# Optimization experiments

Measured on AMD Instinct MI355X. Metric: run time of the kernel, lower is better.

## Reference

```python
import jax, jax.numpy as jnp
import numpy as np

B, NF, DIM, H, W = 2, 8, 128, 40, 40
HID = 256
INNER = 2 * HID            # expansion=2
QKB = 4                    # qkv_block_size -> head dim
NH = INNER // QKB          # 128 heads
DH = QKB                   # 4


def _layernorm(x, w, b, eps=1e-5):
    mu = x.mean(-1, keepdims=True)
    var = x.var(-1, keepdims=True)
    return (x - mu) / jnp.sqrt(var + eps) * w + b


def _mlstm(q, k, v, ig, fg):
    # q,k,v: (Bp,NH,S,DH); ig,fg: (Bp,NH,S,1). Parallel stabilized mLSTM.
    S = q.shape[2]
    lfc = jnp.cumsum(jax.nn.log_sigmoid(fg), axis=2)            # (Bp,NH,S,1)
    m = lfc - jnp.swapaxes(lfc, -2, -1)                          # (Bp,NH,S,S): lfc[i]-lfc[j]
    tri = jnp.tril(jnp.ones((S, S), dtype=bool))
    logD = jnp.where(tri, m + jnp.swapaxes(ig, -2, -1), -jnp.inf)
    maxD = jnp.max(logD, axis=-1, keepdims=True)
    Dm = jnp.exp(logD - maxD)
    qk = jnp.einsum('bnsd,bntd->bnst', q, k) / jnp.sqrt(jnp.asarray(DH, q.dtype))
    C = qk * Dm
    normalizer = jnp.maximum(jnp.abs(C.sum(-1, keepdims=True)), jnp.exp(-maxD))
    return jnp.einsum('bnst,bntd->bnsd', C / (normalizer + 1e-6), v)


def _vil_layer(x, up_w, up_b, conv_w, conv_b, q_w, k_w, ig_w, ig_b, fg_w, fg_b, onorm_w, onorm_b, skip, down_w, down_b):
    Bp, S, _ = x.shape
    xz = x @ up_w.T + up_b                                       # (Bp,S,2*INNER)
    xm, z = jnp.split(xz, 2, axis=-1)
    # causal depthwise conv1d, kernel 4, left pad 3
    xc = jax.lax.conv_general_dilated(jnp.swapaxes(xm, 1, 2), conv_w[:, None, :], (1,), [(3, 0)],
                                      dimension_numbers=('NCH', 'OIH', 'NCH'), feature_group_count=INNER)
    xa = jax.nn.silu(jnp.swapaxes(xc, 1, 2) + conv_b)            # (Bp,S,INNER)
    xah = xa.reshape(Bp, S, NH, DH)
    qh = jnp.einsum('bsnd,ned->bsne', xah, q_w)                  # headwise linear (no bias)
    kh = jnp.einsum('bsnd,ned->bsne', xah, k_w)
    gate_in = jnp.concatenate([qh.reshape(Bp, S, INNER), kh.reshape(Bp, S, INNER), xm], axis=-1)
    ig = jnp.swapaxes(gate_in @ ig_w.T + ig_b, 1, 2)[..., None]  # (Bp,NH,S,1)
    fg = jnp.swapaxes(gate_in @ fg_w.T + fg_b, 1, 2)[..., None]
    q = jnp.swapaxes(qh, 1, 2)
    k = jnp.swapaxes(kh, 1, 2)
    v = jnp.swapaxes(xm.reshape(Bp, S, NH, DH), 1, 2)
    h = _mlstm(q, k, v, ig, fg)                                  # (Bp,NH,S,DH)
    mu = h.mean(-1, keepdims=True)
    var = h.var(-1, keepdims=True)
    hn = (h - mu) / jnp.sqrt(var + 1e-5) * onorm_w.reshape(NH, DH)[None, :, None, :] + onorm_b.reshape(NH, DH)[None, :, None, :]
    h_flat = jnp.swapaxes(hn, 1, 2).reshape(Bp, S, INNER)
    hs = h_flat + skip * xa
    return (hs * jax.nn.silu(z)) @ down_w.T + down_b


def _forward(x, in_fc1_w, in_fc1_b, in_fc2_w, in_fc2_b, out_fc1_w, out_fc1_b, out_fc2_w, out_fc2_b,
             norm_w, norm_b, up_w, up_b, conv_w, conv_b, q_w, k_w, ig_w, ig_b, fg_w, fg_b,
             onorm_w, onorm_b, skip, down_w, down_b):
    Bv, nf, C, Hh, Ww = x.shape
    x_flat = jnp.transpose(x, (0, 3, 4, 1, 2)).reshape(Bv * Hh * Ww, nf, C)
    h = jax.nn.gelu(x_flat @ in_fc1_w.T + in_fc1_b, approximate=False)
    h = h @ in_fc2_w.T + in_fc2_b
    # ViLBlockPair: forward-direction block then backward (flipped) block, each pre-LN residual
    for i, flip in ((0, False), (1, True)):
        y = _layernorm(h, norm_w[i], norm_b[i])
        if flip:
            y = y[:, ::-1]
        y = _vil_layer(y, up_w[i], up_b[i], conv_w[i], conv_b[i], q_w[i], k_w[i], ig_w[i], ig_b[i],
                       fg_w[i], fg_b[i], onorm_w[i], onorm_b[i], skip[i], down_w[i], down_b[i])
        if flip:
            y = y[:, ::-1]
        h = h + y
    o = jax.nn.gelu(h @ out_fc1_w.T + out_fc1_b, approximate=False)
    o = o @ out_fc2_w.T + out_fc2_b
    out = x_flat + o
    return jnp.transpose(out.reshape(Bv, Hh, Ww, nf, C), (0, 3, 4, 1, 2))


def setup_inputs() -> dict:
    key = jax.random.key(0)
    ks = jax.random.split(key, 16)

    def rn(k, shape, std=0.02):
        return jax.random.normal(k, shape, jnp.float32) * std

    return {
        'x': jax.random.normal(ks[0], (B, NF, DIM, H, W), jnp.float32),
        'in_fc1_w': rn(ks[1], (DIM, DIM)), 'in_fc1_b': jnp.zeros((DIM,), jnp.float32),
        'in_fc2_w': rn(ks[2], (HID, DIM)), 'in_fc2_b': jnp.zeros((HID,), jnp.float32),
        'out_fc1_w': rn(ks[3], (HID, HID)), 'out_fc1_b': jnp.zeros((HID,), jnp.float32),
        'out_fc2_w': rn(ks[4], (DIM, HID)), 'out_fc2_b': jnp.zeros((DIM,), jnp.float32),
        'norm_w': jnp.ones((2, HID), jnp.float32), 'norm_b': jnp.zeros((2, HID), jnp.float32),
        'up_w': rn(ks[5], (2, 2 * INNER, HID)), 'up_b': jnp.zeros((2, 2 * INNER), jnp.float32),
        'conv_w': rn(ks[6], (2, INNER, 4), 0.1), 'conv_b': jnp.zeros((2, INNER), jnp.float32),
        'q_w': rn(ks[7], (2, NH, DH, DH), 0.1), 'k_w': rn(ks[8], (2, NH, DH, DH), 0.1),
        'ig_w': rn(ks[9], (2, NH, 3 * INNER), 0.01), 'ig_b': rn(ks[10], (2, NH), 0.1),
        'fg_w': rn(ks[11], (2, NH, 3 * INNER), 0.01),
        'fg_b': jnp.tile(jnp.linspace(3.0, 6.0, NH, dtype=jnp.float32)[None], (2, 1)),
        'onorm_w': jnp.ones((2, INNER), jnp.float32), 'onorm_b': jnp.zeros((2, INNER), jnp.float32),
        'skip': jnp.ones((2, INNER), jnp.float32),
        'down_w': rn(ks[12], (2, HID, INNER)), 'down_b': jnp.zeros((2, HID), jnp.float32),
    }


def reference(x, in_fc1_w, in_fc1_b, in_fc2_w, in_fc2_b, out_fc1_w, out_fc1_b, out_fc2_w, out_fc2_b,
              norm_w, norm_b, up_w, up_b, conv_w, conv_b, q_w, k_w, ig_w, ig_b, fg_w, fg_b,
              onorm_w, onorm_b, skip, down_w, down_b):
    return _forward(x, in_fc1_w, in_fc1_b, in_fc2_w, in_fc2_b, out_fc1_w, out_fc1_b, out_fc2_w, out_fc2_b,
                    norm_w, norm_b, up_w, up_b, conv_w, conv_b, q_w, k_w, ig_w, ig_b, fg_w, fg_b,
                    onorm_w, onorm_b, skip, down_w, down_b)
```

## Files before the change

### kernel.cpp

```cpp
#include <hip/hip_runtime.h>
#include <cstddef>
#include <cstdint>


#define NPOS 3200
#define MTOK 25600

typedef __attribute__((ext_vector_type(8))) short short8;
typedef __attribute__((ext_vector_type(8))) unsigned short u16x8;
typedef __attribute__((ext_vector_type(4))) float f32x4;

__device__ __forceinline__ float bf2f(unsigned short u) {
  union { uint32_t i; float f; } v; v.i = ((uint32_t)u) << 16; return v.f;
}
__device__ __forceinline__ unsigned short f2bf(float f) {
  union { float f; uint32_t i; } v; v.f = f;
  uint32_t r = (v.i + 0x7fffu + ((v.i >> 16) & 1u)) >> 16;
  return (unsigned short)r;
}
__device__ __forceinline__ float geluf(float x) {
  return 0.5f * x * (1.0f + erff(x * 0.70710678118654752f));
}
__device__ __forceinline__ float fast_rcp(float x) { return __builtin_amdgcn_rcpf(x); }
__device__ __forceinline__ float silu_fast(float x) {
  return x * fast_rcp(1.0f + __expf(-x));
}

#define OFF_FC1 0
#define OFF_FC2 16384
#define OFF_OFC1 49152
#define OFF_OFC2 114688
#define OFF_UP 147456
#define OFF_DW 671744
#define OFF_GW 933888
#define WB_ELEMS 1458176

__global__ __launch_bounds__(256) void wprep(const float* __restrict__ fc1w,
                                             const float* __restrict__ fc2w,
                                             const float* __restrict__ ofc1w,
                                             const float* __restrict__ ofc2w,
                                             const float* __restrict__ upw,
                                             const float* __restrict__ dww,
                                             const float* __restrict__ igw,
                                             const float* __restrict__ fgw,
                                             const float* __restrict__ qw,
                                             const float* __restrict__ kw,
                                             const float* __restrict__ igbias,
                                             const float* __restrict__ fgbias,
                                             unsigned short* __restrict__ wb,
                                             float* __restrict__ gbias) {
  int i = blockIdx.x * 256 + threadIdx.x;
  if (i < 16384) { wb[OFF_FC1 + i] = f2bf(fc1w[i]); return; }
  i -= 16384;
  if (i < 32768) { wb[OFF_FC2 + i] = f2bf(fc2w[i]); return; }
  i -= 32768;
  if (i < 65536) { wb[OFF_OFC1 + i] = f2bf(ofc1w[i]); return; }
  i -= 65536;
  if (i < 32768) { wb[OFF_OFC2 + i] = f2bf(ofc2w[i]); return; }
  i -= 32768;
  if (i < 524288) { wb[OFF_UP + i] = f2bf(upw[i]); return; }
  i -= 524288;
  if (i < 262144) { wb[OFF_DW + i] = f2bf(dww[i]); return; }
  i -= 262144;
  if (i < 262144) {
    const int l = i >> 17;
    const int r = i & 131071;
    const int gate = r >> 16;
    const int rr = r & 65535;
    const int row = rr >> 9, c = rr & 511;
    const float* src = (gate ? fgw : igw) + (size_t)l * 196608 + (size_t)row * 1536 + 1024 + c;
    wb[OFF_GW + (size_t)l * 262144 + (size_t)(gate * 128 + row) * 1024 + 512 + c] = f2bf(*src);
    return;
  }
  i -= 262144;
  if (i < 131072) {
    const int l = i >> 16;
    const int r = i & 65535;
    const int jj = r >> 9, c = r & 511;
    const int n = c >> 2, d = c & 3;
    const float* igp = igw + (size_t)l * 196608;
    const float* fgp = fgw + (size_t)l * 196608;
    const float* qp = qw + l * 2048;
    const float* kp = kw + l * 2048;
    float si = 0.f, sf = 0.f;
#pragma unroll
    for (int e = 0; e < 4; ++e) {
      const float qv = qp[n * 16 + e * 4 + d];
      const float kv = kp[n * 16 + e * 4 + d];
      si += igp[jj * 1536 + n * 4 + e] * qv + igp[jj * 1536 + 512 + n * 4 + e] * kv;
      sf += fgp[jj * 1536 + n * 4 + e] * qv + fgp[jj * 1536 + 512 + n * 4 + e] * kv;
    }
    wb[OFF_GW + (size_t)l * 262144 + (size_t)jj * 1024 + c] = f2bf(si);
    wb[OFF_GW + (size_t)l * 262144 + (size_t)(128 + jj) * 1024 + c] = f2bf(sf);
    return;
  }
  i -= 131072;
  if (i < 512) {
    const int l = i >> 8, c = i & 255;
    gbias[l * 256 + c] = (c < 128) ? igbias[l * 128 + c] : fgbias[l * 128 + c - 128];
  }
}

__global__ __launch_bounds__(256) void trans_in(const float* __restrict__ x,
                                                unsigned short* __restrict__ xf) {
  __shared__ float tile[32][33];
  const int b = blockIdx.z;
  const int hw0 = blockIdx.x * 32;
  const int sc0 = blockIdx.y * 32;
  const int tx = threadIdx.x, ty = threadIdx.y;
#pragma unroll
  for (int i = 0; i < 32; i += 8)
    tile[ty + i][tx] = x[((size_t)b * 1024 + sc0 + ty + i) * 1600 + hw0 + tx];
  __syncthreads();
#pragma unroll
  for (int i = 0; i < 32; i += 8)
    xf[((size_t)b * 1600 + hw0 + ty + i) * 1024 + sc0 + tx] = f2bf(tile[tx][ty + i]);
}

__global__ __launch_bounds__(256) void trans_out(const float* __restrict__ x,
                                                 const unsigned short* __restrict__ o,
                                                 float* __restrict__ out) {
  __shared__ float tile[32][33];
  const int b = blockIdx.z;
  const int hw0 = blockIdx.x * 32;
  const int sc0 = blockIdx.y * 32;
  const int tx = threadIdx.x, ty = threadIdx.y;
#pragma unroll
  for (int i = 0; i < 32; i += 8)
    tile[ty + i][tx] = bf2f(o[((size_t)b * 1600 + hw0 + ty + i) * 1024 + sc0 + tx]);
  __syncthreads();
#pragma unroll
  for (int i = 0; i < 32; i += 8) {
    size_t idx = ((size_t)b * 1024 + sc0 + ty + i) * 1600 + hw0 + tx;
    out[idx] = x[idx] + tile[tx][ty + i];
  }
}

template <int MODE>
__global__ __launch_bounds__(256) void mgemm(const unsigned short* __restrict__ A, int lda,
                                             const unsigned short* __restrict__ A2, int lda2,
                                             int KA,
                                             const unsigned short* __restrict__ W, int ldw,
                                             const float* __restrict__ bias,
                                             const float* __restrict__ Cin,
                                             void* __restrict__ Cv, int ldc, int K,
                                             int flip) {
  __shared__ __align__(16) unsigned short Als[2][4][128][8];
  __shared__ __align__(16) unsigned short Bls[2][4][128][8];
  const int t = threadIdx.x;
  const int lane = t & 63, wid = t >> 6;
  const int wr = wid >> 1, wc = wid & 1;
  const int nwg = gridDim.x * gridDim.y;
  const int bid = blockIdx.y * gridDim.x + blockIdx.x;
  const int q = nwg >> 3, r = nwg & 7;
  const int xcd = bid & 7, idx = bid >> 3;
  const int swz = (xcd < r ? xcd * (q + 1) : r * (q + 1) + (xcd - r) * q) + idx;
  const int bx = swz & (gridDim.x - 1);
  const int by = swz >> (31 - __builtin_clz(gridDim.x));
  const int bm = by * 128, bn = bx * 128;
  const int srow = t >> 1;
  const int skh = (t & 1) << 4;
  const int ch = skh >> 3;
  const int kc = lane >> 4;
  const int lr = lane & 15;
  f32x4 acc[4][4] = {};
  const unsigned short* Wp = W + (size_t)(bn + srow) * ldw + skh;

  auto gload = [&](int k0, u16x8& a0, u16x8& a1, u16x8& b0, u16x8& b1) {
    const unsigned short* Ab;
    int kk, ldA;
    if (k0 < KA) { Ab = A; kk = k0; ldA = lda; }
    else { Ab = A2; kk = k0 - KA; ldA = lda2; }
    const unsigned short* ap = Ab + (size_t)(bm + srow) * ldA + kk + skh;
    a0 = *(const u16x8*)ap;
    a1 = *(const u16x8*)(ap + 8);
    b0 = *(const u16x8*)(Wp + k0);
    b1 = *(const u16x8*)(Wp + k0 + 8);
  };
  auto swrite = [&](int buf, u16x8 a0, u16x8 a1, u16x8 b0, u16x8 b1) {
    *(u16x8*)&Als[buf][ch][srow][0] = a0;
    *(u16x8*)&Als[buf][ch + 1][srow][0] = a1;
    *(u16x8*)&Bls[buf][ch][srow][0] = b0;
    *(u16x8*)&Bls[buf][ch + 1][srow][0] = b1;
  };

  u16x8 ca0, ca1, cb0, cb1;
  gload(0, ca0, ca1, cb0, cb1);
  swrite(0, ca0, ca1, cb0, cb1);
  if (K > 32) gload(32, ca0, ca1, cb0, cb1);
  __syncthreads();
  int cur = 0;
  for (int k0 = 0; k0 < K; k0 += 32) {
    u16x8 na0, na1, nb0, nb1;
    if (k0 + 64 < K) gload(k0 + 64, na0, na1, nb0, nb1);
    short8 af[4], bf[4];
#pragma unroll
    for (int mi = 0; mi < 4; ++mi)
      af[mi] = *(const short8*)&Als[cur][kc][wr * 64 + mi * 16 + lr][0];
#pragma unroll
    for (int ni = 0; ni < 4; ++ni)
      bf[ni] = *(const short8*)&Bls[cur][kc][wc * 64 + ni * 16 + lr][0];
#pragma unroll
    for (int mi = 0; mi < 4; ++mi)
#pragma unroll
      for (int ni = 0; ni < 4; ++ni)
        acc[mi][ni] = __builtin_amdgcn_mfma_f32_16x16x32_bf16(af[mi], bf[ni], acc[mi][ni], 0, 0, 0);
    if (k0 + 32 < K) swrite(cur ^ 1, ca0, ca1, cb0, cb1);
    __syncthreads();
    ca0 = na0; ca1 = na1; cb0 = nb0; cb1 = nb1;
    cur ^= 1;
  }

#pragma unroll
  for (int mi = 0; mi < 4; ++mi) {
#pragma unroll
    for (int j = 0; j < 4; ++j) {
      const int m = bm + wr * 64 + mi * 16 + (lane >> 4) * 4 + j;
#pragma unroll
      for (int ni = 0; ni < 4; ++ni) {
        const int col = bn + wc * 64 + ni * 16 + lr;
        float v = acc[mi][ni][j] + bias[col];
        if (MODE == 1) v = geluf(v);
        if (MODE == 0 || MODE == 1) {
          ((unsigned short*)Cv)[(size_t)m * ldc + col] = f2bf(v);
        } else if (MODE == 4) {
          ((float*)Cv)[(size_t)m * ldc + col] = v;
        } else if (MODE == 2) {
          const int pq = m >> 3, s = m & 7;
          const int fs = flip ? (7 - s) : s;
          ((float*)Cv)[(size_t)(pq * 8 + fs) * ldc + col] += v;
        } else {
          const int pq = m >> 3, s = m & 7;
          const int fs = flip ? (7 - s) : s;
          const size_t ix = (size_t)(pq * 8 + fs) * ldc + col;
          ((unsigned short*)Cv)[ix] = f2bf(Cin[ix] + v);
        }
      }
    }
  }
}

__global__ __launch_bounds__(256) void ln_k(const float* __restrict__ h,
                                            const float* __restrict__ w,
                                            const float* __restrict__ b,
                                            unsigned short* __restrict__ y, int flip) {
  const int m = blockIdx.x * 4 + (threadIdx.x >> 6);
  const int lane = threadIdx.x & 63;
  const int p = m >> 3, s = m & 7;
  const int ss = flip ? (7 - s) : s;
  const float* row = h + (size_t)(p * 8 + ss) * 256;
  float4 v = *(const float4*)(row + lane * 4);
  float sum = v.x + v.y + v.z + v.w;
  float sq = v.x * v.x + v.y * v.y + v.z * v.z + v.w * v.w;
#pragma unroll
  for (int o = 32; o > 0; o >>= 1) {
    sum += __shfl_xor(sum, o);
    sq += __shfl_xor(sq, o);
  }
  float mu = sum * (1.f / 256.f);
  float var = sq * (1.f / 256.f) - mu * mu;
  float r = rsqrtf(var + 1e-5f);
  float4 wv = *(const float4*)(w + lane * 4);
  float4 bv = *(const float4*)(b + lane * 4);
  ushort4 o_;
  o_.x = f2bf((v.x - mu) * r * wv.x + bv.x);
  o_.y = f2bf((v.y - mu) * r * wv.y + bv.y);
  o_.z = f2bf((v.z - mu) * r * wv.z + bv.z);
  o_.w = f2bf((v.w - mu) * r * wv.w + bv.w);
  *(ushort4*)(y + (size_t)m * 256 + lane * 4) = o_;
}

__global__ __launch_bounds__(512) void conv_k(const unsigned short* __restrict__ xz,
                                              const float* __restrict__ cw,
                                              const float* __restrict__ cb,
                                              unsigned short* __restrict__ xa) {
  const int p = blockIdx.x;
  const int c = threadIdx.x;
  float v[8];
#pragma unroll
  for (int s = 0; s < 8; ++s) v[s] = bf2f(xz[(size_t)(p * 8 + s) * 1024 + c]);
  const float4 cwv = *(const float4*)(cw + c * 4);
  const float cbv = cb[c];
#pragma unroll
  for (int s = 0; s < 8; ++s) {
    float acc = cbv + v[s] * cwv.w;
    if (s >= 1) acc += v[s - 1] * cwv.z;
    if (s >= 2) acc += v[s - 2] * cwv.y;
    if (s >= 3) acc += v[s - 3] * cwv.x;
    xa[(size_t)(p * 8 + s) * 512 + c] = f2bf(silu_fast(acc));
  }
}

__global__ __launch_bounds__(256) void mlstm_k(unsigned short* __restrict__ xab,
                                               const unsigned short* __restrict__ xz,
                                               const unsigned short* __restrict__ gateb,
                                               const float* __restrict__ qw,
                                               const float* __restrict__ kw,
                                               const float* __restrict__ onw,
                                               const float* __restrict__ onb,
                                               const float* __restrict__ skp) {
  const int p = blockIdx.x * 2 + (threadIdx.x >> 7);
  const int n = threadIdx.x & 127;
  float qwv[4][4], kwv[4][4];
#pragma unroll
  for (int e = 0; e < 4; ++e) {
    float4 q4 = *(const float4*)(qw + n * 16 + e * 4);
    float4 k4 = *(const float4*)(kw + n * 16 + e * 4);
    qwv[e][0] = q4.x; qwv[e][1] = q4.y; qwv[e][2] = q4.z; qwv[e][3] = q4.w;
    kwv[e][0] = k4.x; kwv[e][1] = k4.y; kwv[e][2] = k4.z; kwv[e][3] = k4.w;
  }
  float xa[8][4], k[8][4], v[8][4], lfc[8], ig[8];
  float run = 0.f;
#pragma unroll
  for (int s = 0; s < 8; ++s) {
    const size_t row = (size_t)(p * 8 + s);
    ushort4 xa4 = *(const ushort4*)(xab + row * 512 + n * 4);
    xa[s][0] = bf2f(xa4.x); xa[s][1] = bf2f(xa4.y); xa[s][2] = bf2f(xa4.z); xa[s][3] = bf2f(xa4.w);
    ushort4 v4 = *(const ushort4*)(xz + row * 1024 + n * 4);
    v[s][0] = bf2f(v4.x); v[s][1] = bf2f(v4.y); v[s][2] = bf2f(v4.z); v[s][3] = bf2f(v4.w);
#pragma unroll
    for (int e = 0; e < 4; ++e)
      k[s][e] = xa[s][0] * kwv[e][0] + xa[s][1] * kwv[e][1] + xa[s][2] * kwv[e][2] + xa[s][3] * kwv[e][3];
    ig[s] = bf2f(gateb[row * 256 + n]);
    const float f = bf2f(gateb[row * 256 + 128 + n]);
    const float ls = fminf(f, 0.f) - __logf(1.0f + __expf(-fabsf(f)));
    run += ls;
    lfc[s] = run;
  }
  const float4 onwv = *(const float4*)(onw + n * 4);
  const float4 onbv = *(const float4*)(onb + n * 4);
  const float4 skv = *(const float4*)(skp + n * 4);
#pragma unroll
  for (int s = 0; s < 8; ++s) {
    float q0, q1, q2, q3;
    q0 = xa[s][0] * qwv[0][0] + xa[s][1] * qwv[0][1] + xa[s][2] * qwv[0][2] + xa[s][3] * qwv[0][3];
    q1 = xa[s][0] * qwv[1][0] + xa[s][1] * qwv[1][1] + xa[s][2] * qwv[1][2] + xa[s][3] * qwv[1][3];
    q2 = xa[s][0] * qwv[2][0] + xa[s][1] * qwv[2][1] + xa[s][2] * qwv[2][2] + xa[s][3] * qwv[2][3];
    q3 = xa[s][0] * qwv[3][0] + xa[s][1] * qwv[3][1] + xa[s][2] * qwv[3][2] + xa[s][3] * qwv[3][3];
    float mx = -1e30f;
#pragma unroll
    for (int t = 0; t < 8; ++t)
      if (t <= s) mx = fmaxf(mx, lfc[s] - lfc[t] + ig[t]);
    float csum = 0.f;
    float o0 = 0, o1 = 0, o2 = 0, o3 = 0;
#pragma unroll
    for (int t = 0; t < 8; ++t)
      if (t <= s) {
        const float dm = __expf(lfc[s] - lfc[t] + ig[t] - mx);
        const float qkd = (q0 * k[t][0] + q1 * k[t][1] + q2 * k[t][2] + q3 * k[t][3]) * 0.5f;
        const float cc = qkd * dm;
        csum += cc;
        o0 += cc * v[t][0]; o1 += cc * v[t][1]; o2 += cc * v[t][2]; o3 += cc * v[t][3];
      }
    const float inv = fast_rcp(fmaxf(fabsf(csum), __expf(-mx)) + 1e-6f);
    o0 *= inv; o1 *= inv; o2 *= inv; o3 *= inv;
    const float mu = 0.25f * (o0 + o1 + o2 + o3);
    const float d0 = o0 - mu, d1 = o1 - mu, d2 = o2 - mu, d3 = o3 - mu;
    const float var = 0.25f * (d0 * d0 + d1 * d1 + d2 * d2 + d3 * d3);
    const float r = __builtin_amdgcn_rsqf(var + 1e-5f);
    const size_t row = (size_t)(p * 8 + s);
    ushort4 z4 = *(const ushort4*)(xz + row * 1024 + 512 + n * 4);
    ushort4 ge;
    ge.x = f2bf((d0 * r * onwv.x + onbv.x + skv.x * xa[s][0]) * silu_fast(bf2f(z4.x)));
    ge.y = f2bf((d1 * r * onwv.y + onbv.y + skv.y * xa[s][1]) * silu_fast(bf2f(z4.y)));
    ge.z = f2bf((d2 * r * onwv.z + onbv.z + skv.z * xa[s][2]) * silu_fast(bf2f(z4.z)));
    ge.w = f2bf((d3 * r * onwv.w + onbv.w + skv.w * xa[s][3]) * silu_fast(bf2f(z4.w)));
    *(ushort4*)(xab + row * 512 + n * 4) = ge;
  }
}

extern "C" void kernel_launch(void* const* d_in, const int* in_sizes, int n_in,
                              void* d_out, int out_size, void* d_ws, size_t ws_size,
                              hipStream_t stream) {
  const float* x = (const float*)d_in[0];
  const float* fc1w = (const float*)d_in[1];
  const float* fc1b = (const float*)d_in[2];
  const float* fc2w = (const float*)d_in[3];
  const float* fc2b = (const float*)d_in[4];
  const float* ofc1w = (const float*)d_in[5];
  const float* ofc1b = (const float*)d_in[6];
  const float* ofc2w = (const float*)d_in[7];
  const float* ofc2b = (const float*)d_in[8];
  const float* nw = (const float*)d_in[9];
  const float* nb = (const float*)d_in[10];
  const float* upw = (const float*)d_in[11];
  const float* upb = (const float*)d_in[12];
  const float* cw = (const float*)d_in[13];
  const float* cb = (const float*)d_in[14];
  const float* qw = (const float*)d_in[15];
  const float* kw = (const float*)d_in[16];
  const float* igw = (const float*)d_in[17];
  const float* igbias = (const float*)d_in[18];
  const float* fgw = (const float*)d_in[19];
  const float* fgbias = (const float*)d_in[20];
  const float* onw = (const float*)d_in[21];
  const float* onb = (const float*)d_in[22];
  const float* skp = (const float*)d_in[23];
  const float* dww = (const float*)d_in[24];
  const float* dwb = (const float*)d_in[25];
  float* out = (float*)d_out;

  char* ws = (char*)d_ws;
  float* hbuf = (float*)ws;
  unsigned short* bufD = (unsigned short*)(ws + 26214400);
  unsigned short* bufA = (unsigned short*)(ws + 39321600);
  unsigned short* xz = (unsigned short*)(ws + 45875200);
  unsigned short* hmirror = xz;
  unsigned short* xab = (unsigned short*)(ws + 98304000);
  unsigned short* xflat = xab;
  unsigned short* wb = (unsigned short*)(ws + 124518400);
  float* gbias = (float*)(ws + 124518400 + 2916352);

  wprep<<<dim3(5186), 256, 0, stream>>>(fc1w, fc2w, ofc1w, ofc2w, upw, dww, igw, fgw, qw, kw,
                                        igbias, fgbias, wb, gbias);

  dim3 tb(32, 8);
  trans_in<<<dim3(50, 32, 2), tb, 0, stream>>>(x, xflat);
  mgemm<1><<<dim3(1, 200), 256, 0, stream>>>(xflat, 128, xflat, 128, 128, wb + OFF_FC1, 128,
                                             fc1b, nullptr, bufA, 128, 128, 0);
  mgemm<4><<<dim3(2, 200), 256, 0, stream>>>(bufA, 128, bufA, 128, 128, wb + OFF_FC2, 128,
                                             fc2b, nullptr, hbuf, 256, 128, 0);

  for (int i = 0; i < 2; ++i) {
    ln_k<<<dim3(6400), 256, 0, stream>>>(hbuf, nw + i * 256, nb + i * 256, bufD, i);
    mgemm<0><<<dim3(8, 200), 256, 0, stream>>>(bufD, 256, bufD, 256, 256,
                                               wb + OFF_UP + (size_t)i * 262144, 256,
                                               upb + i * 1024, nullptr, xz, 1024, 256, 0);
    conv_k<<<dim3(NPOS), 512, 0, stream>>>(xz, cw + i * 2048, cb + i * 512, xab);
    mgemm<0><<<dim3(2, 200), 256, 0, stream>>>(xab, 512, xz, 1024, 512,
                                               wb + OFF_GW + (size_t)i * 262144, 1024,
                                               gbias + i * 256, nullptr, bufD, 256, 1024, 0);
    mlstm_k<<<dim3(1600), 256, 0, stream>>>(xab, xz, bufD, qw + i * 2048, kw + i * 2048,
                                            onw + i * 512, onb + i * 512, skp + i * 512);
    if (i == 0) {
      mgemm<2><<<dim3(2, 200), 256, 0, stream>>>(xab, 512, xab, 512, 512, wb + OFF_DW, 512,
                                                 dwb, nullptr, hbuf, 256, 512, 0);
    } else {
      mgemm<6><<<dim3(2, 200), 256, 0, stream>>>(xab, 512, xab, 512, 512, wb + OFF_DW + 131072,
                                                 512, dwb + 256, hbuf, hmirror, 256, 512, 1);
    }
  }

  mgemm<1><<<dim3(2, 200), 256, 0, stream>>>(hmirror, 256, hmirror, 256, 256, wb + OFF_OFC1, 256,
                                             ofc1b, nullptr, bufD, 256, 256, 0);
  mgemm<0><<<dim3(1, 200), 256, 0, stream>>>(bufD, 256, bufD, 256, 256, wb + OFF_OFC2, 256,
                                             ofc2b, nullptr, bufA, 128, 256, 0);
  trans_out<<<dim3(50, 32, 2), tb, 0, stream>>>(x, bufA, out);
}
```

Measured before the change: 305.0 us.

## Store residual stream in bf16, interleave gate rows, recompute conv in mLSTM

The fp32 residual buffer becomes bf16, which halves the traffic for the fc2 output, the LayerNorm reads and the down-projection accumulate. The ig and fg gate weight rows and biases are interleaved so mlstm_k reads both gates with one ushort2 load. mlstm_k now recomputes the causal depthwise conv and SiLU from xz instead of reading xab. The bf16 residual accumulation across layers loses precision, and recomputing the conv adds arithmetic in mlstm_k.

```diff
diff --git a/kernel.cpp b/kernel.cpp
--- a/kernel.cpp
+++ b/kernel.cpp
@@ -69,7 +69,7 @@
     const int rr = r & 65535;
     const int row = rr >> 9, c = rr & 511;
     const float* src = (gate ? fgw : igw) + (size_t)l * 196608 + (size_t)row * 1536 + 1024 + c;
-    wb[OFF_GW + (size_t)l * 262144 + (size_t)(gate * 128 + row) * 1024 + 512 + c] = f2bf(*src);
+    wb[OFF_GW + (size_t)l * 262144 + (size_t)(2 * row + gate) * 1024 + 512 + c] = f2bf(*src);
     return;
   }
   i -= 262144;
@@ -90,14 +90,14 @@
       si += igp[jj * 1536 + n * 4 + e] * qv + igp[jj * 1536 + 512 + n * 4 + e] * kv;
       sf += fgp[jj * 1536 + n * 4 + e] * qv + fgp[jj * 1536 + 512 + n * 4 + e] * kv;
     }
-    wb[OFF_GW + (size_t)l * 262144 + (size_t)jj * 1024 + c] = f2bf(si);
-    wb[OFF_GW + (size_t)l * 262144 + (size_t)(128 + jj) * 1024 + c] = f2bf(sf);
+    wb[OFF_GW + (size_t)l * 262144 + (size_t)(2 * jj) * 1024 + c] = f2bf(si);
+    wb[OFF_GW + (size_t)l * 262144 + (size_t)(2 * jj + 1) * 1024 + c] = f2bf(sf);
     return;
   }
   i -= 131072;
   if (i < 512) {
     const int l = i >> 8, c = i & 255;
-    gbias[l * 256 + c] = (c < 128) ? igbias[l * 128 + c] : fgbias[l * 128 + c - 128];
+    gbias[l * 256 + c] = (c & 1) ? fgbias[l * 128 + (c >> 1)] : igbias[l * 128 + (c >> 1)];
   }
 }
 
@@ -142,7 +142,7 @@
                                              int KA,
                                              const unsigned short* __restrict__ W, int ldw,
                                              const float* __restrict__ bias,
-                                             const float* __restrict__ Cin,
+                                             const unsigned short* __restrict__ Cin,
                                              void* __restrict__ Cv, int ldc, int K,
                                              int flip) {
   __shared__ __align__(16) unsigned short Als[2][4][128][8];
@@ -223,24 +223,23 @@
         if (MODE == 1) v = geluf(v);
         if (MODE == 0 || MODE == 1) {
           ((unsigned short*)Cv)[(size_t)m * ldc + col] = f2bf(v);
-        } else if (MODE == 4) {
-          ((float*)Cv)[(size_t)m * ldc + col] = v;
         } else if (MODE == 2) {
           const int pq = m >> 3, s = m & 7;
           const int fs = flip ? (7 - s) : s;
-          ((float*)Cv)[(size_t)(pq * 8 + fs) * ldc + col] += v;
+          unsigned short* p = (unsigned short*)Cv + (size_t)(pq * 8 + fs) * ldc + col;
+          *p = f2bf(bf2f(*p) + v);
         } else {
           const int pq = m >> 3, s = m & 7;
           const int fs = flip ? (7 - s) : s;
           const size_t ix = (size_t)(pq * 8 + fs) * ldc + col;
-          ((unsigned short*)Cv)[ix] = f2bf(Cin[ix] + v);
+          ((unsigned short*)Cv)[ix] = f2bf(bf2f(Cin[ix]) + v);
         }
       }
     }
   }
 }
 
-__global__ __launch_bounds__(256) void ln_k(const float* __restrict__ h,
+__global__ __launch_bounds__(256) void ln_k(const unsigned short* __restrict__ h,
                                             const float* __restrict__ w,
                                             const float* __restrict__ b,
                                             unsigned short* __restrict__ y, int flip) {
@@ -248,10 +247,11 @@
   const int lane = threadIdx.x & 63;
   const int p = m >> 3, s = m & 7;
   const int ss = flip ? (7 - s) : s;
-  const float* row = h + (size_t)(p * 8 + ss) * 256;
-  float4 v = *(const float4*)(row + lane * 4);
-  float sum = v.x + v.y + v.z + v.w;
-  float sq = v.x * v.x + v.y * v.y + v.z * v.z + v.w * v.w;
+  const unsigned short* row = h + (size_t)(p * 8 + ss) * 256;
+  ushort4 u4 = *(const ushort4*)(row + lane * 4);
+  float v0 = bf2f(u4.x), v1 = bf2f(u4.y), v2 = bf2f(u4.z), v3 = bf2f(u4.w);
+  float sum = v0 + v1 + v2 + v3;
+  float sq = v0 * v0 + v1 * v1 + v2 * v2 + v3 * v3;
 #pragma unroll
   for (int o = 32; o > 0; o >>= 1) {
     sum += __shfl_xor(sum, o);
@@ -263,10 +263,10 @@
   float4 wv = *(const float4*)(w + lane * 4);
   float4 bv = *(const float4*)(b + lane * 4);
   ushort4 o_;
-  o_.x = f2bf((v.x - mu) * r * wv.x + bv.x);
-  o_.y = f2bf((v.y - mu) * r * wv.y + bv.y);
-  o_.z = f2bf((v.z - mu) * r * wv.z + bv.z);
-  o_.w = f2bf((v.w - mu) * r * wv.w + bv.w);
+  o_.x = f2bf((v0 - mu) * r * wv.x + bv.x);
+  o_.y = f2bf((v1 - mu) * r * wv.y + bv.y);
+  o_.z = f2bf((v2 - mu) * r * wv.z + bv.z);
+  o_.w = f2bf((v3 - mu) * r * wv.w + bv.w);
   *(ushort4*)(y + (size_t)m * 256 + lane * 4) = o_;
 }
 
@@ -294,6 +294,8 @@
 __global__ __launch_bounds__(256) void mlstm_k(unsigned short* __restrict__ xab,
                                                const unsigned short* __restrict__ xz,
                                                const unsigned short* __restrict__ gateb,
+                                               const float* __restrict__ cw,
+                                               const float* __restrict__ cb,
                                                const float* __restrict__ qw,
                                                const float* __restrict__ kw,
                                                const float* __restrict__ onw,
@@ -301,31 +303,49 @@
                                                const float* __restrict__ skp) {
   const int p = blockIdx.x * 2 + (threadIdx.x >> 7);
   const int n = threadIdx.x & 127;
-  float qwv[4][4], kwv[4][4];
+  float kwv[4][4], cwt[4][4];
+  float cbv[4];
 #pragma unroll
   for (int e = 0; e < 4; ++e) {
-    float4 q4 = *(const float4*)(qw + n * 16 + e * 4);
     float4 k4 = *(const float4*)(kw + n * 16 + e * 4);
-    qwv[e][0] = q4.x; qwv[e][1] = q4.y; qwv[e][2] = q4.z; qwv[e][3] = q4.w;
     kwv[e][0] = k4.x; kwv[e][1] = k4.y; kwv[e][2] = k4.z; kwv[e][3] = k4.w;
+    float4 c4 = *(const float4*)(cw + (n * 4 + e) * 4);
+    cwt[e][0] = c4.x; cwt[e][1] = c4.y; cwt[e][2] = c4.z; cwt[e][3] = c4.w;
+  }
+  {
+    float4 cb4 = *(const float4*)(cb + n * 4);
+    cbv[0] = cb4.x; cbv[1] = cb4.y; cbv[2] = cb4.z; cbv[3] = cb4.w;
   }
   float xa[8][4], k[8][4], v[8][4], lfc[8], ig[8];
   float run = 0.f;
 #pragma unroll
   for (int s = 0; s < 8; ++s) {
     const size_t row = (size_t)(p * 8 + s);
-    ushort4 xa4 = *(const ushort4*)(xab + row * 512 + n * 4);
-    xa[s][0] = bf2f(xa4.x); xa[s][1] = bf2f(xa4.y); xa[s][2] = bf2f(xa4.z); xa[s][3] = bf2f(xa4.w);
     ushort4 v4 = *(const ushort4*)(xz + row * 1024 + n * 4);
     v[s][0] = bf2f(v4.x); v[s][1] = bf2f(v4.y); v[s][2] = bf2f(v4.z); v[s][3] = bf2f(v4.w);
 #pragma unroll
+    for (int e = 0; e < 4; ++e) {
+      float a = cbv[e] + v[s][e] * cwt[e][3];
+      if (s >= 1) a += v[s - 1][e] * cwt[e][2];
+      if (s >= 2) a += v[s - 2][e] * cwt[e][1];
+      if (s >= 3) a += v[s - 3][e] * cwt[e][0];
+      xa[s][e] = bf2f(f2bf(silu_fast(a)));
+    }
+#pragma unroll
     for (int e = 0; e < 4; ++e)
       k[s][e] = xa[s][0] * kwv[e][0] + xa[s][1] * kwv[e][1] + xa[s][2] * kwv[e][2] + xa[s][3] * kwv[e][3];
-    ig[s] = bf2f(gateb[row * 256 + n]);
-    const float f = bf2f(gateb[row * 256 + 128 + n]);
+    const ushort2 g2 = *(const ushort2*)(gateb + row * 256 + n * 2);
+    ig[s] = bf2f(g2.x);
+    const float f = bf2f(g2.y);
     const float ls = fminf(f, 0.f) - __logf(1.0f + __expf(-fabsf(f)));
     run += ls;
     lfc[s] = run;
+  }
+  float qwv[4][4];
+#pragma unroll
+  for (int e = 0; e < 4; ++e) {
+    float4 q4 = *(const float4*)(qw + n * 16 + e * 4);
+    qwv[e][0] = q4.x; qwv[e][1] = q4.y; qwv[e][2] = q4.z; qwv[e][3] = q4.w;
   }
   const float4 onwv = *(const float4*)(onw + n * 4);
   const float4 onbv = *(const float4*)(onb + n * 4);
@@ -401,15 +421,15 @@
   float* out = (float*)d_out;
 
   char* ws = (char*)d_ws;
-  float* hbuf = (float*)ws;
-  unsigned short* bufD = (unsigned short*)(ws + 26214400);
-  unsigned short* bufA = (unsigned short*)(ws + 39321600);
-  unsigned short* xz = (unsigned short*)(ws + 45875200);
+  unsigned short* hbuf = (unsigned short*)ws;
+  unsigned short* bufD = (unsigned short*)(ws + 13107200);
+  unsigned short* bufA = (unsigned short*)(ws + 26214400);
+  unsigned short* xz = (unsigned short*)(ws + 32768000);
   unsigned short* hmirror = xz;
-  unsigned short* xab = (unsigned short*)(ws + 98304000);
+  unsigned short* xab = (unsigned short*)(ws + 85196800);
   unsigned short* xflat = xab;
-  unsigned short* wb = (unsigned short*)(ws + 124518400);
-  float* gbias = (float*)(ws + 124518400 + 2916352);
+  unsigned short* wb = (unsigned short*)(ws + 111411200);
+  float* gbias = (float*)(ws + 111411200 + 2916352);
 
   wprep<<<dim3(5186), 256, 0, stream>>>(fc1w, fc2w, ofc1w, ofc2w, upw, dww, igw, fgw, qw, kw,
                                         igbias, fgbias, wb, gbias);
@@ -418,7 +438,7 @@
   trans_in<<<dim3(50, 32, 2), tb, 0, stream>>>(x, xflat);
   mgemm<1><<<dim3(1, 200), 256, 0, stream>>>(xflat, 128, xflat, 128, 128, wb + OFF_FC1, 128,
                                              fc1b, nullptr, bufA, 128, 128, 0);
-  mgemm<4><<<dim3(2, 200), 256, 0, stream>>>(bufA, 128, bufA, 128, 128, wb + OFF_FC2, 128,
+  mgemm<0><<<dim3(2, 200), 256, 0, stream>>>(bufA, 128, bufA, 128, 128, wb + OFF_FC2, 128,
                                              fc2b, nullptr, hbuf, 256, 128, 0);
 
   for (int i = 0; i < 2; ++i) {
@@ -430,7 +450,8 @@
     mgemm<0><<<dim3(2, 200), 256, 0, stream>>>(xab, 512, xz, 1024, 512,
                                                wb + OFF_GW + (size_t)i * 262144, 1024,
                                                gbias + i * 256, nullptr, bufD, 256, 1024, 0);
-    mlstm_k<<<dim3(1600), 256, 0, stream>>>(xab, xz, bufD, qw + i * 2048, kw + i * 2048,
+    mlstm_k<<<dim3(1600), 256, 0, stream>>>(xab, xz, bufD, cw + i * 2048, cb + i * 512,
+                                            qw + i * 2048, kw + i * 2048,
                                             onw + i * 512, onb + i * 512, skp + i * 512);
     if (i == 0) {
       mgemm<2><<<dim3(2, 200), 256, 0, stream>>>(xab, 512, xab, 512, 512, wb + OFF_DW, 512,
```

Result: no change. 304.7 us (-0.1%).
